# Performance work log

Hardware: AMD Instinct MI355X
Metric: run time of the kernel (lower is better)

Reference implementation:

```python
import jax, jax.numpy as jnp
import numpy as np

H = 1024   # hidden_dim
D = 256    # output_dim
T = 64     # output_len
B = 256    # batch
FC1, FC2 = 1024, 512
EPS = 1e-5


def setup_inputs() -> dict:
    key = jax.random.key(0)
    ks = iter(jax.random.split(key, 32))
    s = 0.05
    p = {}
    p['hidden'] = jax.random.normal(next(ks), (2, B, H), jnp.float32)
    # GRU layer 0: input D -> hidden H ; layer 1: H -> H
    p['W_ih0'] = jax.random.normal(next(ks), (3 * H, D), jnp.float32) * s
    p['W_hh0'] = jax.random.normal(next(ks), (3 * H, H), jnp.float32) * s
    p['b_ih0'] = jax.random.normal(next(ks), (3 * H,), jnp.float32) * s
    p['b_hh0'] = jax.random.normal(next(ks), (3 * H,), jnp.float32) * s
    p['W_ih1'] = jax.random.normal(next(ks), (3 * H, H), jnp.float32) * s
    p['W_hh1'] = jax.random.normal(next(ks), (3 * H, H), jnp.float32) * s
    p['b_ih1'] = jax.random.normal(next(ks), (3 * H,), jnp.float32) * s
    p['b_hh1'] = jax.random.normal(next(ks), (3 * H,), jnp.float32) * s
    # FC head: H -> 1024 -> 512 -> D
    p['fc1_w'] = jax.random.normal(next(ks), (FC1, H), jnp.float32) * s
    p['fc1_b'] = jnp.zeros((FC1,), jnp.float32)
    p['ln1_g'] = jnp.ones((FC1,), jnp.float32)
    p['ln1_b'] = jnp.zeros((FC1,), jnp.float32)
    p['fc2_w'] = jax.random.normal(next(ks), (FC2, FC1), jnp.float32) * s
    p['fc2_b'] = jnp.zeros((FC2,), jnp.float32)
    p['ln2_g'] = jnp.ones((FC2,), jnp.float32)
    p['ln2_b'] = jnp.zeros((FC2,), jnp.float32)
    p['fc3_w'] = jax.random.normal(next(ks), (D, FC2), jnp.float32) * s
    p['fc3_b'] = jnp.zeros((D,), jnp.float32)
    return p


def _gru_cell(x, h, W_ih, W_hh, b_ih, b_hh):
    gi = x @ W_ih.T + b_ih            # [B, 3H]
    gh = h @ W_hh.T + b_hh            # [B, 3H]
    i_r, i_z, i_n = jnp.split(gi, 3, axis=-1)
    h_r, h_z, h_n = jnp.split(gh, 3, axis=-1)
    r = jax.nn.sigmoid(i_r + h_r)
    z = jax.nn.sigmoid(i_z + h_z)
    n = jnp.tanh(i_n + r * h_n)
    return (1.0 - z) * n + z * h


def _layernorm(x, g, b):
    mu = jnp.mean(x, axis=-1, keepdims=True)
    var = jnp.mean(jnp.square(x - mu), axis=-1, keepdims=True)
    return (x - mu) * jax.lax.rsqrt(var + EPS) * g + b


def reference(hidden, W_ih0, W_hh0, b_ih0, b_hh0, W_ih1, W_hh1, b_ih1, b_hh1,
              fc1_w, fc1_b, ln1_g, ln1_b, fc2_w, fc2_b, ln2_g, ln2_b, fc3_w, fc3_b):
    batch = hidden.shape[1]

    def fc_head(x):
        x = jax.nn.gelu(_layernorm(x @ fc1_w.T + fc1_b, ln1_g, ln1_b), approximate=False)
        x = jax.nn.gelu(_layernorm(x @ fc2_w.T + fc2_b, ln2_g, ln2_b), approximate=False)
        return x @ fc3_w.T + fc3_b

    def step(carry, _):
        h0, h1, out = carry
        h0 = _gru_cell(out, h0, W_ih0, W_hh0, b_ih0, b_hh0)
        h1 = _gru_cell(h0, h1, W_ih1, W_hh1, b_ih1, b_hh1)
        out = jax.nn.softmax(fc_head(h1), axis=-1)   # fed back as next input
        return (h0, h1, out), out

    init = (hidden[0], hidden[1], jnp.zeros((batch, D), hidden.dtype))
    _, outs = jax.lax.scan(step, init, None, length=T)   # [T, B, D]
    return jnp.transpose(outs, (1, 0, 2))                # [B, T, D]
```

## Files before the change

kernel.cpp:

```cpp
#include <hip/hip_runtime.h>
#include <math.h>

typedef __bf16 bf16_t;
typedef __bf16 bf16x8 __attribute__((ext_vector_type(8)));
typedef float f32x4 __attribute__((ext_vector_type(4)));

#define B_ 256
#define H_ 1024

template<int NW, int EPI>
__global__ __launch_bounds__(NW * 64) void gemm_mfma(
    const bf16_t* __restrict__ A, const bf16_t* __restrict__ W,
    const float* __restrict__ bias, int K,
    float* __restrict__ C, int ldc,
    float* __restrict__ hf,
    bf16_t* __restrict__ d1, int ld1, int off1,
    bf16_t* __restrict__ d2, int ld2, int off2)
{
    constexpr int MT = NW * 16;
    constexpr int R = 4 / NW;
    __shared__ __align__(16) bf16_t ldsA[2][2][MT * 40];
    __shared__ __align__(16) bf16_t ldsB[2][2][64 * 40];

    int bx = blockIdx.x, by = blockIdx.y;
    if (EPI == 1) {
        int d = by * 64 + bx;
        bx = (d & 7) * 8 + ((d >> 3) & 7);
        by = d >> 6;
    }
    const int bm = by * MT, bn = bx * 64;
    const int tid = threadIdx.x;

    const int srow = tid >> 2, schk = tid & 3;
    const bf16_t* gA = A + (size_t)(bm + srow) * K + schk * 8;
    const bf16_t* gW = W + (size_t)(bn + srow) * K + schk * 8;
    const unsigned sa = srow * 40 + schk * 8;

    const int lane = tid & 63, wv = tid >> 6;
    const int quad = lane >> 4, col = lane & 15;
    const unsigned ra_off = (wv * 16 + col) * 40 + quad * 8;
    const unsigned rb_off = col * 40 + quad * 8;

    f32x4 acc[4];
#pragma unroll
    for (int j = 0; j < 4; j++)
#pragma unroll
        for (int e = 0; e < 4; e++) acc[j][e] = 0.f;

    int4 pa0, pa1, pb0[R], pb1[R];

    pa0 = *(const int4*)gA;
    pa1 = *(const int4*)(gA + 32);
#pragma unroll
    for (int r = 0; r < R; r++) {
        pb0[r] = *(const int4*)(gW + (size_t)(r * MT) * K);
        pb1[r] = *(const int4*)(gW + (size_t)(r * MT) * K + 32);
    }
    gA += 64; gW += 64;

    *(int4*)&ldsA[0][0][sa] = pa0;
    *(int4*)&ldsA[0][1][sa] = pa1;
#pragma unroll
    for (int r = 0; r < R; r++) {
        *(int4*)&ldsB[0][0][sa + r * MT * 40] = pb0[r];
        *(int4*)&ldsB[0][1][sa + r * MT * 40] = pb1[r];
    }

    pa0 = *(const int4*)gA;
    pa1 = *(const int4*)(gA + 32);
#pragma unroll
    for (int r = 0; r < R; r++) {
        pb0[r] = *(const int4*)(gW + (size_t)(r * MT) * K);
        pb1[r] = *(const int4*)(gW + (size_t)(r * MT) * K + 32);
    }
    gA += 64; gW += 64;

    const int nit = K >> 6;
    __syncthreads();

    for (int c = 0; c < nit; ++c) {
        const int cur = c & 1;
        bf16x8 af0 = *(const bf16x8*)&ldsA[cur][0][ra_off];
        bf16x8 af1 = *(const bf16x8*)&ldsA[cur][1][ra_off];
        bf16x8 b00 = *(const bf16x8*)&ldsB[cur][0][rb_off];
        bf16x8 b01 = *(const bf16x8*)&ldsB[cur][0][rb_off + 16 * 40];
        bf16x8 b02 = *(const bf16x8*)&ldsB[cur][0][rb_off + 32 * 40];
        bf16x8 b03 = *(const bf16x8*)&ldsB[cur][0][rb_off + 48 * 40];
        bf16x8 b10 = *(const bf16x8*)&ldsB[cur][1][rb_off];
        bf16x8 b11 = *(const bf16x8*)&ldsB[cur][1][rb_off + 16 * 40];
        bf16x8 b12 = *(const bf16x8*)&ldsB[cur][1][rb_off + 32 * 40];
        bf16x8 b13 = *(const bf16x8*)&ldsB[cur][1][rb_off + 48 * 40];

        if (c + 1 < nit) {
            const int nxt = cur ^ 1;
            *(int4*)&ldsA[nxt][0][sa] = pa0;
            *(int4*)&ldsA[nxt][1][sa] = pa1;
#pragma unroll
            for (int r = 0; r < R; r++) {
                *(int4*)&ldsB[nxt][0][sa + r * MT * 40] = pb0[r];
                *(int4*)&ldsB[nxt][1][sa + r * MT * 40] = pb1[r];
            }
            if (c + 2 < nit) {
                pa0 = *(const int4*)gA;
                pa1 = *(const int4*)(gA + 32);
#pragma unroll
                for (int r = 0; r < R; r++) {
                    pb0[r] = *(const int4*)(gW + (size_t)(r * MT) * K);
                    pb1[r] = *(const int4*)(gW + (size_t)(r * MT) * K + 32);
                }
                gA += 64; gW += 64;
            }
        }

        acc[0] = __builtin_amdgcn_mfma_f32_16x16x32_bf16(af0, b00, acc[0], 0, 0, 0);
        acc[1] = __builtin_amdgcn_mfma_f32_16x16x32_bf16(af0, b01, acc[1], 0, 0, 0);
        acc[2] = __builtin_amdgcn_mfma_f32_16x16x32_bf16(af0, b02, acc[2], 0, 0, 0);
        acc[3] = __builtin_amdgcn_mfma_f32_16x16x32_bf16(af0, b03, acc[3], 0, 0, 0);
        acc[0] = __builtin_amdgcn_mfma_f32_16x16x32_bf16(af1, b10, acc[0], 0, 0, 0);
        acc[1] = __builtin_amdgcn_mfma_f32_16x16x32_bf16(af1, b11, acc[1], 0, 0, 0);
        acc[2] = __builtin_amdgcn_mfma_f32_16x16x32_bf16(af1, b12, acc[2], 0, 0, 0);
        acc[3] = __builtin_amdgcn_mfma_f32_16x16x32_bf16(af1, b13, acc[3], 0, 0, 0);

        __syncthreads();
    }

    if (EPI == 0) {
#pragma unroll
        for (int j = 0; j < 4; j++) {
            const int n = bn + j * 16 + col;
            const float bj = bias[n];
#pragma unroll
            for (int r = 0; r < 4; r++) {
                const int m = bm + wv * 16 + quad * 4 + r;
                C[(size_t)m * ldc + n] = acc[j][r] + bj;
            }
        }
    } else {
        const int cch = (bn >> 2) + col;
        const float br  = bias[bn + col];
        const float bz  = bias[bn + 16 + col];
        const float bin = bias[bn + 32 + col];
        const float bhn = bias[bn + 48 + col];
#pragma unroll
        for (int r = 0; r < 4; r++) {
            const int m = bm + wv * 16 + quad * 4 + r;
            const float gr  = acc[0][r] + br;
            const float gz  = acc[1][r] + bz;
            const float gin = acc[2][r] + bin;
            const float ghn = acc[3][r] + bhn;
            const float rr = 1.f / (1.f + __expf(-gr));
            const float zz = 1.f / (1.f + __expf(-gz));
            const float nn = tanhf(gin + rr * ghn);
            const size_t hidx = (size_t)m * 1024 + cch;
            const float hnew = (1.f - zz) * nn + zz * hf[hidx];
            hf[hidx] = hnew;
            const bf16_t hb = (bf16_t)hnew;
            d1[(size_t)m * ld1 + off1 + cch] = hb;
            d2[(size_t)m * ld2 + off2 + cch] = hb;
        }
    }
}

__global__ __launch_bounds__(256) void build_w4(
    const float* __restrict__ Wih, const float* __restrict__ Whh,
    const float* __restrict__ bih, const float* __restrict__ bhh,
    bf16_t* __restrict__ W4, float* __restrict__ b4, int Kx)
{
    const int K = Kx + 1024;
    const int tpr = K >> 2;
    const int idx = blockIdx.x * 256 + threadIdx.x;
    const int np = idx / tpr;
    const int k4 = (idx - np * tpr) * 4;
    const int c = ((np >> 6) << 4) + (np & 15);
    const int g = (np >> 4) & 3;
    const int srow = (g == 0 ? c : (g == 1 ? 1024 + c : 2048 + c));
    float4 v = make_float4(0.f, 0.f, 0.f, 0.f);
    if (k4 < Kx) {
        if (g != 3) v = *(const float4*)(Wih + (size_t)srow * Kx + k4);
    } else {
        if (g != 2) v = *(const float4*)(Whh + (size_t)srow * 1024 + (k4 - Kx));
    }
    bf16_t* dst = W4 + (size_t)np * K + k4;
    dst[0] = (bf16_t)v.x; dst[1] = (bf16_t)v.y;
    dst[2] = (bf16_t)v.z; dst[3] = (bf16_t)v.w;
    if (k4 == 0) {
        b4[np] = (g == 0) ? bih[c] + bhh[c]
               : (g == 1) ? bih[1024 + c] + bhh[1024 + c]
               : (g == 2) ? bih[2048 + c] : bhh[2048 + c];
    }
}

__global__ __launch_bounds__(256) void conv_bf16(
    const float* __restrict__ src, bf16_t* __restrict__ dst)
{
    const int i4 = (blockIdx.x * 256 + threadIdx.x) * 4;
    float4 v = *(const float4*)(src + i4);
    dst[i4 + 0] = (bf16_t)v.x; dst[i4 + 1] = (bf16_t)v.y;
    dst[i4 + 2] = (bf16_t)v.z; dst[i4 + 3] = (bf16_t)v.w;
}

__global__ __launch_bounds__(256) void init_state(
    const float* __restrict__ hidden, float* __restrict__ h0f,
    float* __restrict__ h1f, bf16_t* __restrict__ A0_0, bf16_t* __restrict__ A1_0)
{
    const int i = blockIdx.x * 256 + threadIdx.x;
    const int m = i >> 10, c = i & 1023;
    const float h0 = hidden[i], h1 = hidden[262144 + i];
    h0f[i] = h0; h1f[i] = h1;
    A0_0[(size_t)m * 1280 + 256 + c] = (bf16_t)h0;
    A1_0[(size_t)m * 2048 + 1024 + c] = (bf16_t)h1;
    if (c < 256) A0_0[(size_t)m * 1280 + c] = (bf16_t)0.f;
}

__device__ __forceinline__ float block_reduce_sum(float v, float* red)
{
#pragma unroll
    for (int o = 32; o > 0; o >>= 1) v += __shfl_xor(v, o, 64);
    const int wid = threadIdx.x >> 6;
    if ((threadIdx.x & 63) == 0) red[wid] = v;
    __syncthreads();
    float s = red[0] + red[1] + red[2] + red[3];
    __syncthreads();
    return s;
}

template <int N>
__global__ __launch_bounds__(256) void ln_gelu(
    const float* __restrict__ X, const float* __restrict__ g,
    const float* __restrict__ b, bf16_t* __restrict__ Y)
{
    __shared__ float red[4];
    const int row = blockIdx.x;
    const int tid = threadIdx.x;
    constexpr int PT = N / 256;
    float v[PT];
    float s = 0.f;
#pragma unroll
    for (int i = 0; i < PT; i++) {
        v[i] = X[(size_t)row * N + tid + i * 256];
        s += v[i];
    }
    const float mu = block_reduce_sum(s, red) * (1.f / N);
    float s2 = 0.f;
#pragma unroll
    for (int i = 0; i < PT; i++) { float d = v[i] - mu; s2 += d * d; }
    const float var = block_reduce_sum(s2, red) * (1.f / N);
    const float inv = rsqrtf(var + 1e-5f);
#pragma unroll
    for (int i = 0; i < PT; i++) {
        const int c = tid + i * 256;
        const float t = (v[i] - mu) * inv * g[c] + b[c];
        Y[(size_t)row * N + c] = (bf16_t)(0.5f * t * (1.f + erff(t * 0.70710678118654752f)));
    }
}

__global__ __launch_bounds__(256) void softmax_fb(
    const float* __restrict__ logits, float* __restrict__ dout,
    bf16_t* __restrict__ a0w, int t)
{
    const int wv = threadIdx.x >> 6, lane = threadIdx.x & 63;
    const int row = blockIdx.x * 4 + wv;
    float v[4];
#pragma unroll
    for (int j = 0; j < 4; j++) v[j] = logits[(size_t)row * 256 + lane + 64 * j];
    float mx = fmaxf(fmaxf(v[0], v[1]), fmaxf(v[2], v[3]));
#pragma unroll
    for (int o = 32; o > 0; o >>= 1) mx = fmaxf(mx, __shfl_xor(mx, o, 64));
    float e[4], s = 0.f;
#pragma unroll
    for (int j = 0; j < 4; j++) { e[j] = expf(v[j] - mx); s += e[j]; }
#pragma unroll
    for (int o = 32; o > 0; o >>= 1) s += __shfl_xor(s, o, 64);
    const float inv = 1.f / s;
#pragma unroll
    for (int j = 0; j < 4; j++) {
        const float p = e[j] * inv;
        const int c = lane + 64 * j;
        dout[((size_t)row * 64 + t) * 256 + c] = p;
        a0w[(size_t)row * 1280 + c] = (bf16_t)p;
    }
}

extern "C" void kernel_launch(void* const* d_in, const int* in_sizes, int n_in,
                              void* d_out, int out_size, void* d_ws, size_t ws_size,
                              hipStream_t stream)
{
    const float* hidden = (const float*)d_in[0];
    const float* W_ih0  = (const float*)d_in[1];
    const float* W_hh0  = (const float*)d_in[2];
    const float* b_ih0  = (const float*)d_in[3];
    const float* b_hh0  = (const float*)d_in[4];
    const float* W_ih1  = (const float*)d_in[5];
    const float* W_hh1  = (const float*)d_in[6];
    const float* b_ih1  = (const float*)d_in[7];
    const float* b_hh1  = (const float*)d_in[8];
    const float* fc1_w  = (const float*)d_in[9];
    const float* fc1_b  = (const float*)d_in[10];
    const float* ln1_g  = (const float*)d_in[11];
    const float* ln1_b  = (const float*)d_in[12];
    const float* fc2_w  = (const float*)d_in[13];
    const float* fc2_b  = (const float*)d_in[14];
    const float* ln2_g  = (const float*)d_in[15];
    const float* ln2_b  = (const float*)d_in[16];
    const float* fc3_w  = (const float*)d_in[17];
    const float* fc3_b  = (const float*)d_in[18];
    float* dout = (float*)d_out;

    char* p = (char*)d_ws;
    auto alloc = [&](size_t bytes) { void* r = (void*)p; p += (bytes + 255) & ~(size_t)255; return r; };
    float*  h0f   = (float*)alloc(262144 * 4);
    float*  h1f   = (float*)alloc(262144 * 4);
    bf16_t* A0[2] = { (bf16_t*)alloc(256 * 1280 * 2), (bf16_t*)alloc(256 * 1280 * 2) };
    bf16_t* A1[2] = { (bf16_t*)alloc(256 * 2048 * 2), (bf16_t*)alloc(256 * 2048 * 2) };
    bf16_t* h1b   = (bf16_t*)alloc(262144 * 2);
    float*  a1r   = (float*)alloc(262144 * 4);
    bf16_t* a1b   = (bf16_t*)alloc(262144 * 2);
    float*  a2r   = (float*)alloc(131072 * 4);
    bf16_t* a2b   = (bf16_t*)alloc(131072 * 2);
    float*  logits= (float*)alloc(65536 * 4);
    float*  b4_0  = (float*)alloc(4096 * 4);
    float*  b4_1  = (float*)alloc(4096 * 4);
    bf16_t* W4_0  = (bf16_t*)alloc((size_t)4096 * 1280 * 2);
    bf16_t* W4_1  = (bf16_t*)alloc((size_t)4096 * 2048 * 2);
    bf16_t* fc1wb = (bf16_t*)alloc((size_t)1048576 * 2);
    bf16_t* fc2wb = (bf16_t*)alloc((size_t)524288 * 2);
    bf16_t* fc3wb = (bf16_t*)alloc((size_t)131072 * 2);

    build_w4<<<5120, 256, 0, stream>>>(W_ih0, W_hh0, b_ih0, b_hh0, W4_0, b4_0, 256);
    build_w4<<<8192, 256, 0, stream>>>(W_ih1, W_hh1, b_ih1, b_hh1, W4_1, b4_1, 1024);
    conv_bf16<<<1024, 256, 0, stream>>>(fc1_w, fc1wb);
    conv_bf16<<<512, 256, 0, stream>>>(fc2_w, fc2wb);
    conv_bf16<<<128, 256, 0, stream>>>(fc3_w, fc3wb);
    init_state<<<1024, 256, 0, stream>>>(hidden, h0f, h1f, A0[0], A1[0]);

    for (int t = 0; t < 64; t++) {
        bf16_t* A0r = A0[t & 1];
        bf16_t* A0w = A0[(t + 1) & 1];
        bf16_t* A1r = A1[t & 1];
        bf16_t* A1w = A1[(t + 1) & 1];

        gemm_mfma<4, 1><<<dim3(64, 4), 256, 0, stream>>>(
            A0r, W4_0, b4_0, 1280, nullptr, 0,
            h0f, A1r, 2048, 0, A0w, 1280, 256);
        gemm_mfma<4, 1><<<dim3(64, 4), 256, 0, stream>>>(
            A1r, W4_1, b4_1, 2048, nullptr, 0,
            h1f, A1w, 2048, 1024, h1b, 1024, 0);
        gemm_mfma<2, 0><<<dim3(16, 8), 128, 0, stream>>>(
            h1b, fc1wb, fc1_b, 1024, a1r, 1024, nullptr, nullptr, 0, 0, nullptr, 0, 0);
        ln_gelu<1024><<<256, 256, 0, stream>>>(a1r, ln1_g, ln1_b, a1b);
        gemm_mfma<2, 0><<<dim3(8, 8), 128, 0, stream>>>(
            a1b, fc2wb, fc2_b, 1024, a2r, 512, nullptr, nullptr, 0, 0, nullptr, 0, 0);
        ln_gelu<512><<<256, 256, 0, stream>>>(a2r, ln2_g, ln2_b, a2b);
        gemm_mfma<2, 0><<<dim3(4, 8), 128, 0, stream>>>(
            a2b, fc3wb, fc3_b, 512, logits, 256, nullptr, nullptr, 0, 0, nullptr, 0, 0);
        softmax_fb<<<64, 256, 0, stream>>>(logits, dout, A0w, t);
    }
}
```

Before: 4.652 ms.

## Fuse LayerNorm+GELU prologue into following FC GEMMs, dropping separate ln_gelu kernels

Replaces the standalone ln_gelu kernels and bf16 intermediate buffers with a GEMM whose prologue computes per-row mean and variance from fp32 pre-activations. It then applies LN+GELU while staging A tiles into LDS. This removes two kernel launches per timestep and one round trip through global memory. In exchange, each block recomputes row statistics redundantly and evaluates erf in the load path. Variance now uses the E[x^2]-mu^2 form, which changes numerics slightly.

```diff
diff --git a/kernel.cpp b/kernel.cpp
--- a/kernel.cpp
+++ b/kernel.cpp
@@ -161,6 +161,178 @@
     }
 }
 
+__device__ __forceinline__ bf16_t ln_gelu_one(float x, float mu, float inv,
+                                              float g, float b)
+{
+    const float t = (x - mu) * inv * g + b;
+    return (bf16_t)(0.5f * t * (1.f + erff(t * 0.70710678118654752f)));
+}
+
+__device__ __forceinline__ int4 pack8(float4 xl, float4 xh, float4 gl, float4 gh,
+                                      float4 bl, float4 bh, float mu, float inv)
+{
+    union { bf16_t e[8]; int4 q; } u;
+    u.e[0] = ln_gelu_one(xl.x, mu, inv, gl.x, bl.x);
+    u.e[1] = ln_gelu_one(xl.y, mu, inv, gl.y, bl.y);
+    u.e[2] = ln_gelu_one(xl.z, mu, inv, gl.z, bl.z);
+    u.e[3] = ln_gelu_one(xl.w, mu, inv, gl.w, bl.w);
+    u.e[4] = ln_gelu_one(xh.x, mu, inv, gh.x, bh.x);
+    u.e[5] = ln_gelu_one(xh.y, mu, inv, gh.y, bh.y);
+    u.e[6] = ln_gelu_one(xh.z, mu, inv, gh.z, bh.z);
+    u.e[7] = ln_gelu_one(xh.w, mu, inv, gh.w, bh.w);
+    return u.q;
+}
+
+template<int KN>
+__global__ __launch_bounds__(128) void fc_ln_gemm(
+    const float* __restrict__ X, const float* __restrict__ lng,
+    const float* __restrict__ lnb, const bf16_t* __restrict__ W,
+    const float* __restrict__ bias, float* __restrict__ C, int ldc)
+{
+    __shared__ __align__(16) bf16_t ldsA[2][2][32 * 40];
+    __shared__ __align__(16) bf16_t ldsB[2][2][64 * 40];
+
+    const int bm = blockIdx.y * 32, bn = blockIdx.x * 64;
+    const int tid = threadIdx.x;
+
+    const int srow = tid >> 2, schk = tid & 3;
+    const bf16_t* gW = W + (size_t)(bn + srow) * KN + schk * 8;
+    const unsigned sa = srow * 40 + schk * 8;
+    const float* xrow = X + (size_t)(bm + srow) * KN;
+
+    float mu, inv;
+    {
+        const float* xr = xrow + schk * (KN / 4);
+        float s = 0.f, s2 = 0.f;
+#pragma unroll 8
+        for (int i = 0; i < KN / 16; i++) {
+            float4 v = *(const float4*)(xr + i * 4);
+            s  += v.x + v.y + v.z + v.w;
+            s2 += v.x * v.x + v.y * v.y + v.z * v.z + v.w * v.w;
+        }
+        s  += __shfl_xor(s, 1, 64);  s  += __shfl_xor(s, 2, 64);
+        s2 += __shfl_xor(s2, 1, 64); s2 += __shfl_xor(s2, 2, 64);
+        mu  = s * (1.f / KN);
+        inv = rsqrtf(fmaxf(s2 * (1.f / KN) - mu * mu, 0.f) + 1e-5f);
+    }
+
+    const int lane = tid & 63, wv = tid >> 6;
+    const int quad = lane >> 4, col = lane & 15;
+    const unsigned ra_off = ((wv & 1) * 16 + col) * 40 + quad * 8;
+    const unsigned rb_off = col * 40 + quad * 8;
+
+    f32x4 acc[4];
+#pragma unroll
+    for (int j = 0; j < 4; j++)
+#pragma unroll
+        for (int e = 0; e < 4; e++) acc[j][e] = 0.f;
+
+    const float* xc = xrow + schk * 8;
+    const float* gc = lng + schk * 8;
+    const float* bc = lnb + schk * 8;
+
+    float4 pX0, pX1, pX2, pX3, pG0, pG1, pG2, pG3, pB0, pB1, pB2, pB3;
+    int4 pb0[2], pb1[2];
+
+    pX0 = *(const float4*)(xc);      pX1 = *(const float4*)(xc + 4);
+    pX2 = *(const float4*)(xc + 32); pX3 = *(const float4*)(xc + 36);
+    pG0 = *(const float4*)(gc);      pG1 = *(const float4*)(gc + 4);
+    pG2 = *(const float4*)(gc + 32); pG3 = *(const float4*)(gc + 36);
+    pB0 = *(const float4*)(bc);      pB1 = *(const float4*)(bc + 4);
+    pB2 = *(const float4*)(bc + 32); pB3 = *(const float4*)(bc + 36);
+#pragma unroll
+    for (int r = 0; r < 2; r++) {
+        pb0[r] = *(const int4*)(gW + (size_t)(r * 32) * KN);
+        pb1[r] = *(const int4*)(gW + (size_t)(r * 32) * KN + 32);
+    }
+    xc += 64; gc += 64; bc += 64; gW += 64;
+
+    *(int4*)&ldsA[0][0][sa] = pack8(pX0, pX1, pG0, pG1, pB0, pB1, mu, inv);
+    *(int4*)&ldsA[0][1][sa] = pack8(pX2, pX3, pG2, pG3, pB2, pB3, mu, inv);
+#pragma unroll
+    for (int r = 0; r < 2; r++) {
+        *(int4*)&ldsB[0][0][sa + r * 32 * 40] = pb0[r];
+        *(int4*)&ldsB[0][1][sa + r * 32 * 40] = pb1[r];
+    }
+
+    pX0 = *(const float4*)(xc);      pX1 = *(const float4*)(xc + 4);
+    pX2 = *(const float4*)(xc + 32); pX3 = *(const float4*)(xc + 36);
+    pG0 = *(const float4*)(gc);      pG1 = *(const float4*)(gc + 4);
+    pG2 = *(const float4*)(gc + 32); pG3 = *(const float4*)(gc + 36);
+    pB0 = *(const float4*)(bc);      pB1 = *(const float4*)(bc + 4);
+    pB2 = *(const float4*)(bc + 32); pB3 = *(const float4*)(bc + 36);
+#pragma unroll
+    for (int r = 0; r < 2; r++) {
+        pb0[r] = *(const int4*)(gW + (size_t)(r * 32) * KN);
+        pb1[r] = *(const int4*)(gW + (size_t)(r * 32) * KN + 32);
+    }
+    xc += 64; gc += 64; bc += 64; gW += 64;
+
+    const int nit = KN >> 6;
+    __syncthreads();
+
+    for (int c = 0; c < nit; ++c) {
+        const int cur = c & 1;
+        bf16x8 af0 = *(const bf16x8*)&ldsA[cur][0][ra_off];
+        bf16x8 af1 = *(const bf16x8*)&ldsA[cur][1][ra_off];
+        bf16x8 b00 = *(const bf16x8*)&ldsB[cur][0][rb_off];
+        bf16x8 b01 = *(const bf16x8*)&ldsB[cur][0][rb_off + 16 * 40];
+        bf16x8 b02 = *(const bf16x8*)&ldsB[cur][0][rb_off + 32 * 40];
+        bf16x8 b03 = *(const bf16x8*)&ldsB[cur][0][rb_off + 48 * 40];
+        bf16x8 b10 = *(const bf16x8*)&ldsB[cur][1][rb_off];
+        bf16x8 b11 = *(const bf16x8*)&ldsB[cur][1][rb_off + 16 * 40];
+        bf16x8 b12 = *(const bf16x8*)&ldsB[cur][1][rb_off + 32 * 40];
+        bf16x8 b13 = *(const bf16x8*)&ldsB[cur][1][rb_off + 48 * 40];
+
+        if (c + 1 < nit) {
+            const int nxt = cur ^ 1;
+            *(int4*)&ldsA[nxt][0][sa] = pack8(pX0, pX1, pG0, pG1, pB0, pB1, mu, inv);
+            *(int4*)&ldsA[nxt][1][sa] = pack8(pX2, pX3, pG2, pG3, pB2, pB3, mu, inv);
+#pragma unroll
+            for (int r = 0; r < 2; r++) {
+                *(int4*)&ldsB[nxt][0][sa + r * 32 * 40] = pb0[r];
+                *(int4*)&ldsB[nxt][1][sa + r * 32 * 40] = pb1[r];
+            }
+            if (c + 2 < nit) {
+                pX0 = *(const float4*)(xc);      pX1 = *(const float4*)(xc + 4);
+                pX2 = *(const float4*)(xc + 32); pX3 = *(const float4*)(xc + 36);
+                pG0 = *(const float4*)(gc);      pG1 = *(const float4*)(gc + 4);
+                pG2 = *(const float4*)(gc + 32); pG3 = *(const float4*)(gc + 36);
+                pB0 = *(const float4*)(bc);      pB1 = *(const float4*)(bc + 4);
+                pB2 = *(const float4*)(bc + 32); pB3 = *(const float4*)(bc + 36);
+#pragma unroll
+                for (int r = 0; r < 2; r++) {
+                    pb0[r] = *(const int4*)(gW + (size_t)(r * 32) * KN);
+                    pb1[r] = *(const int4*)(gW + (size_t)(r * 32) * KN + 32);
+                }
+                xc += 64; gc += 64; bc += 64; gW += 64;
+            }
+        }
+
+        acc[0] = __builtin_amdgcn_mfma_f32_16x16x32_bf16(af0, b00, acc[0], 0, 0, 0);
+        acc[1] = __builtin_amdgcn_mfma_f32_16x16x32_bf16(af0, b01, acc[1], 0, 0, 0);
+        acc[2] = __builtin_amdgcn_mfma_f32_16x16x32_bf16(af0, b02, acc[2], 0, 0, 0);
+        acc[3] = __builtin_amdgcn_mfma_f32_16x16x32_bf16(af0, b03, acc[3], 0, 0, 0);
+        acc[0] = __builtin_amdgcn_mfma_f32_16x16x32_bf16(af1, b10, acc[0], 0, 0, 0);
+        acc[1] = __builtin_amdgcn_mfma_f32_16x16x32_bf16(af1, b11, acc[1], 0, 0, 0);
+        acc[2] = __builtin_amdgcn_mfma_f32_16x16x32_bf16(af1, b12, acc[2], 0, 0, 0);
+        acc[3] = __builtin_amdgcn_mfma_f32_16x16x32_bf16(af1, b13, acc[3], 0, 0, 0);
+
+        __syncthreads();
+    }
+
+#pragma unroll
+    for (int j = 0; j < 4; j++) {
+        const int n = bn + j * 16 + col;
+        const float bj = bias[n];
+#pragma unroll
+        for (int r = 0; r < 4; r++) {
+            const int m = bm + (wv & 1) * 16 + quad * 4 + r;
+            C[(size_t)m * ldc + n] = acc[j][r] + bj;
+        }
+    }
+}
+
 __global__ __launch_bounds__(256) void build_w4(
     const float* __restrict__ Wih, const float* __restrict__ Whh,
     const float* __restrict__ bih, const float* __restrict__ bhh,
@@ -210,48 +382,6 @@
     A0_0[(size_t)m * 1280 + 256 + c] = (bf16_t)h0;
     A1_0[(size_t)m * 2048 + 1024 + c] = (bf16_t)h1;
     if (c < 256) A0_0[(size_t)m * 1280 + c] = (bf16_t)0.f;
-}
-
-__device__ __forceinline__ float block_reduce_sum(float v, float* red)
-{
-#pragma unroll
-    for (int o = 32; o > 0; o >>= 1) v += __shfl_xor(v, o, 64);
-    const int wid = threadIdx.x >> 6;
-    if ((threadIdx.x & 63) == 0) red[wid] = v;
-    __syncthreads();
-    float s = red[0] + red[1] + red[2] + red[3];
-    __syncthreads();
-    return s;
-}
-
-template <int N>
-__global__ __launch_bounds__(256) void ln_gelu(
-    const float* __restrict__ X, const float* __restrict__ g,
-    const float* __restrict__ b, bf16_t* __restrict__ Y)
-{
-    __shared__ float red[4];
-    const int row = blockIdx.x;
-    const int tid = threadIdx.x;
-    constexpr int PT = N / 256;
-    float v[PT];
-    float s = 0.f;
-#pragma unroll
-    for (int i = 0; i < PT; i++) {
-        v[i] = X[(size_t)row * N + tid + i * 256];
-        s += v[i];
-    }
-    const float mu = block_reduce_sum(s, red) * (1.f / N);
-    float s2 = 0.f;
-#pragma unroll
-    for (int i = 0; i < PT; i++) { float d = v[i] - mu; s2 += d * d; }
-    const float var = block_reduce_sum(s2, red) * (1.f / N);
-    const float inv = rsqrtf(var + 1e-5f);
-#pragma unroll
-    for (int i = 0; i < PT; i++) {
-        const int c = tid + i * 256;
-        const float t = (v[i] - mu) * inv * g[c] + b[c];
-        Y[(size_t)row * N + c] = (bf16_t)(0.5f * t * (1.f + erff(t * 0.70710678118654752f)));
-    }
 }
 
 __global__ __launch_bounds__(256) void softmax_fb(
@@ -314,9 +444,7 @@
     bf16_t* A1[2] = { (bf16_t*)alloc(256 * 2048 * 2), (bf16_t*)alloc(256 * 2048 * 2) };
     bf16_t* h1b   = (bf16_t*)alloc(262144 * 2);
     float*  a1r   = (float*)alloc(262144 * 4);
-    bf16_t* a1b   = (bf16_t*)alloc(262144 * 2);
     float*  a2r   = (float*)alloc(131072 * 4);
-    bf16_t* a2b   = (bf16_t*)alloc(131072 * 2);
     float*  logits= (float*)alloc(65536 * 4);
     float*  b4_0  = (float*)alloc(4096 * 4);
     float*  b4_1  = (float*)alloc(4096 * 4);
@@ -347,12 +475,10 @@
             h1f, A1w, 2048, 1024, h1b, 1024, 0);
         gemm_mfma<2, 0><<<dim3(16, 8), 128, 0, stream>>>(
             h1b, fc1wb, fc1_b, 1024, a1r, 1024, nullptr, nullptr, 0, 0, nullptr, 0, 0);
-        ln_gelu<1024><<<256, 256, 0, stream>>>(a1r, ln1_g, ln1_b, a1b);
-        gemm_mfma<2, 0><<<dim3(8, 8), 128, 0, stream>>>(
-            a1b, fc2wb, fc2_b, 1024, a2r, 512, nullptr, nullptr, 0, 0, nullptr, 0, 0);
-        ln_gelu<512><<<256, 256, 0, stream>>>(a2r, ln2_g, ln2_b, a2b);
-        gemm_mfma<2, 0><<<dim3(4, 8), 128, 0, stream>>>(
-            a2b, fc3wb, fc3_b, 512, logits, 256, nullptr, nullptr, 0, 0, nullptr, 0, 0);
+        fc_ln_gemm<1024><<<dim3(8, 8), 128, 0, stream>>>(
+            a1r, ln1_g, ln1_b, fc2wb, fc2_b, a2r, 512);
+        fc_ln_gemm<512><<<dim3(4, 8), 128, 0, stream>>>(
+            a2r, ln2_g, ln2_b, fc3wb, fc3_b, logits, 256);
         softmax_fb<<<64, 256, 0, stream>>>(logits, dout, A0w, t);
     }
 }
```

New measurement: 7.620 ms. +63.8%, slower.
